# Performance work log

Measured on AMD Instinct MI355X. Metric: run time of the kernel, lower is better.

## Reference

```python
import jax, jax.numpy as jnp
import numpy as np
import math

B, D = 8192, 128
STEEPNESS = 1.0
TOPK_NEG = 10
N_SORT = TOPK_NEG + 1  # n_pos_augs - 1 + topk_neg = 1 + 10
EPS = 1e-8


def setup_inputs() -> dict:
    key = jax.random.key(0)
    k1, k2 = jax.random.split(key)
    aug1 = jax.random.normal(k1, (B, D), dtype=jnp.float32)
    aug2 = jax.random.normal(k2, (B, D), dtype=jnp.float32)
    return {"aug1": aug1, "aug2": aug2}


def _soft_sort_odd_even(x, steepness):
    """Differentiable odd-even transposition sort (diffsort, cauchy interpolation).
    x: [B, n]. Returns (sorted_x [B, n], P [B, n, n]) where sorted_x = x @ P and
    P[i, j] = relaxed probability that input element i lands at sorted position j."""
    b, n = x.shape
    P = jnp.broadcast_to(jnp.eye(n, dtype=x.dtype), (b, n, n))
    for layer in range(n):  # n layers, alternating even/odd pairs
        off = layer % 2
        idx_a = np.arange(off, n - 1, 2)
        idx_b = idx_a + 1
        a = x[:, idx_a]
        bb = x[:, idx_b]
        # cauchy CDF relaxation: alpha -> 1 when b > a (already ordered)
        alpha = jnp.arctan(steepness * (bb - a)) / math.pi + 0.5
        x = x.at[:, idx_a].set(alpha * a + (1.0 - alpha) * bb)
        x = x.at[:, idx_b].set((1.0 - alpha) * a + alpha * bb)
        Pa = P[:, :, idx_a]
        Pb = P[:, :, idx_b]
        al = alpha[:, None, :]
        P = P.at[:, :, idx_a].set(al * Pa + (1.0 - al) * Pb)
        P = P.at[:, :, idx_b].set((1.0 - al) * Pa + al * Pb)
    return x, P


def _bce(p, t):
    # torch.nn.BCELoss with log clamped at -100
    logp = jnp.clip(jnp.log(p), -100.0, None)
    log1mp = jnp.clip(jnp.log(1.0 - p), -100.0, None)
    return -jnp.mean(t * logp + (1.0 - t) * log1mp)


def _compute_loss(anchor, positive):
    anchor = anchor.astype(jnp.float32)
    positive = jax.lax.stop_gradient(positive.astype(jnp.float32))  # stop_grad=True
    # pairwise cosine similarity (dim=1)
    an = anchor / jnp.maximum(jnp.linalg.norm(anchor, axis=1, keepdims=True), EPS)
    pn = positive / jnp.maximum(jnp.linalg.norm(positive, axis=1, keepdims=True), EPS)
    pos_sims = jnp.sum(an * pn, axis=1, keepdims=True)  # [B, 1]; sort over dim=1 is a no-op
    # all-to-all cosine similarity vs detached anchors (negatives = anchor.detach())
    negs = jax.lax.stop_gradient(an)
    sim = an @ negs.T  # [B, B]
    nb = sim.shape[0]
    sim = jnp.where(jnp.eye(nb, dtype=bool), -jnp.inf, sim)  # mask self-similarity
    neg_top, _ = jax.lax.top_k(sim, TOPK_NEG)  # descending
    neg_top = neg_top[:, ::-1]                 # flip -> ascending
    sims = jnp.concatenate([neg_top, pos_sims], axis=1)  # [B, 11]
    _, P = _soft_sort_odd_even(sims, STEEPNESS)
    n = sims.shape[1]
    # perm_target = identity -> column-sum targets are first-k indicators
    p_neg = jnp.clip(jnp.sum(P[:, :, :TOPK_NEG], axis=2), 0.0, 1.0)  # [B, n]
    p_pos = jnp.clip(jnp.sum(P[:, :, TOPK_NEG:], axis=2), 0.0, 1.0)
    t_neg = jnp.broadcast_to((jnp.arange(n) < TOPK_NEG).astype(jnp.float32), (nb, n))
    t_pos = 1.0 - t_neg
    return 0.5 * (_bce(p_pos, t_pos) + _bce(p_neg, t_neg))


def reference(aug1, aug2):
    # n_augs = 2: each aug serves as anchor once, the other as the single positive
    loss1 = _compute_loss(aug1, aug2)
    loss2 = _compute_loss(aug2, aug1)
    return (loss1 + loss2) / 2.0
```

## Files before the change

### kernel.cpp

```cpp
#include <hip/hip_runtime.h>
#include <cstdint>
#include <cmath>

#define NB 8192
#define ND 128
#define CAP 48
#define CAPP 49
#define NEG_INF (-__builtin_inff())

typedef __attribute__((ext_vector_type(8))) __bf16 bf16x8;
typedef __attribute__((ext_vector_type(2))) __bf16 bf16x2;
typedef __attribute__((ext_vector_type(4))) float f32x4;


__device__ __forceinline__ void insert10(float t[10], float v) {
#pragma unroll
  for (int j = 0; j < 9; ++j) t[j] = __builtin_amdgcn_fmed3f(t[j], t[j + 1], v);
  t[9] = fmaxf(t[9], v);
}
__device__ __forceinline__ void insert11(float t[11], float v) {
#pragma unroll
  for (int j = 0; j < 10; ++j) t[j] = __builtin_amdgcn_fmed3f(t[j], t[j + 1], v);
  t[10] = fmaxf(t[10], v);
}

__device__ float row_loss(float x[11]) {
  float al[55];
#pragma unroll
  for (int layer = 0; layer < 11; ++layer) {
#pragma unroll
    for (int p = 0; p < 5; ++p) {
      int ii = (layer & 1) + 2 * p;
      float av = x[ii], bv = x[ii + 1];
      float a = atanf(bv - av) * 0.3183098861837907f + 0.5f;
      al[layer * 5 + p] = a;
      float be = 1.f - a;
      x[ii] = a * av + be * bv;
      x[ii + 1] = be * av + a * bv;
    }
  }
  float v[11];
#pragma unroll
  for (int i = 0; i < 11; ++i) v[i] = 0.f;
  v[10] = 1.f;
#pragma unroll
  for (int layer = 10; layer >= 0; --layer) {
#pragma unroll
    for (int p = 0; p < 5; ++p) {
      int ii = (layer & 1) + 2 * p;
      float a = al[layer * 5 + p];
      float be = 1.f - a;
      float va = v[ii], vb = v[ii + 1];
      v[ii] = a * va + be * vb;
      v[ii + 1] = be * va + a * vb;
    }
  }
  float C = fmaxf(logf(v[10]), -100.f);
#pragma unroll
  for (int i = 0; i < 10; ++i) C += fmaxf(logf(1.f - v[i]), -100.f);
  return C;
}

__global__ __launch_bounds__(256, 4) void knorm(const float* __restrict__ aug1,
                                                const float* __restrict__ aug2,
                                                __bf16* __restrict__ an,
                                                float* __restrict__ pos,
                                                float* __restrict__ out) {
  if (blockIdx.x == 0 && threadIdx.x == 0) out[0] = 0.f;
  int wid = threadIdx.x >> 6;
  int l = threadIdx.x & 63;
  int row = blockIdx.x * 4 + wid;
  const float2* a1 = (const float2*)(aug1) + (size_t)row * 64;
  const float2* a2 = (const float2*)(aug2) + (size_t)row * 64;
  float2 v1 = a1[l], v2 = a2[l];
  float ss1 = v1.x * v1.x + v1.y * v1.y;
  float ss2 = v2.x * v2.x + v2.y * v2.y;
  float dp = v1.x * v2.x + v1.y * v2.y;
#pragma unroll
  for (int off = 1; off < 64; off <<= 1) {
    ss1 += __shfl_xor(ss1, off);
    ss2 += __shfl_xor(ss2, off);
    dp += __shfl_xor(dp, off);
  }
  float inv1 = 1.0f / fmaxf(sqrtf(ss1), 1e-8f);
  float inv2 = 1.0f / fmaxf(sqrtf(ss2), 1e-8f);
  bf16x2 o1, o2;
  o1[0] = (__bf16)(v1.x * inv1);
  o1[1] = (__bf16)(v1.y * inv1);
  o2[0] = (__bf16)(v2.x * inv2);
  o2[1] = (__bf16)(v2.y * inv2);
  int unit = ((row >> 4) << 8) + ((l >> 4) << 6) + (((l >> 2) & 3) << 4) + (row & 15);
  ((bf16x2*)(an))[unit * 4 + (l & 3)] = o1;
  ((bf16x2*)(an + (size_t)NB * ND))[unit * 4 + (l & 3)] = o2;
  if (l == 0) pos[row] = dp * inv1 * inv2;
}

__global__ __launch_bounds__(256, 4) void kgram(const __bf16* __restrict__ an_all,
                                                float* __restrict__ tk,
                                                int* __restrict__ cnth,
                                                float* __restrict__ taug) {
  int dir = blockIdx.y;
  int rowg = blockIdx.x >> 2;
  int quar = blockIdx.x & 3;
  const bf16x8* an8 = (const bf16x8*)(an_all + (size_t)dir * NB * ND);
  int w = threadIdx.x >> 6;
  int l = threadIdx.x & 63;
  int q = l >> 4;
  int c = l & 15;
  int row_base = rowg * 64;
  const int col0 = quar * 2048;

  __shared__ float cand[64][CAPP];
  __shared__ int lcnt[64];
  __shared__ float sred[2][4];
  if (threadIdx.x < 64) lcnt[threadIdx.x] = 0;

  bf16x8 brow[4][4];
#pragma unroll
  for (int rb = 0; rb < 4; ++rb)
#pragma unroll
    for (int kc = 0; kc < 4; ++kc)
      brow[rb][kc] = an8[(size_t)row_base * 16 + rb * 256 + kc * 64 + l];

  const bf16x8* pf0 = an8 + ((size_t)col0 * 16 + w * 256 + l);
  bf16x8 a[4], a2[4];
  const f32x4 zz = {0.f, 0.f, 0.f, 0.f};
  f32x4 accA[4], accB[4];

  auto loadA = [&](int t) {
    const bf16x8* p = pf0 + (size_t)(t & 31) * 1024;
#pragma unroll
    for (int kc = 0; kc < 4; ++kc) a[kc] = p[kc * 64];
  };
  auto loadA2 = [&](int t) {
    const bf16x8* p = pf0 + (size_t)(t & 31) * 1024;
#pragma unroll
    for (int kc = 0; kc < 4; ++kc) a2[kc] = p[kc * 64];
  };
  auto mfma_tile = [&](f32x4* A, const bf16x8* src) {
#pragma unroll
    for (int rb = 0; rb < 4; ++rb)
      A[rb] = __builtin_amdgcn_mfma_f32_16x16x32_bf16(src[0], brow[rb][0], zz, 0, 0, 0);
#pragma unroll
    for (int kc = 1; kc < 4; ++kc)
#pragma unroll
      for (int rb = 0; rb < 4; ++rb)
        A[rb] = __builtin_amdgcn_mfma_f32_16x16x32_bf16(src[kc], brow[rb][kc], A[rb], 0, 0, 0);
  };
  auto consume = [&](const f32x4* acc, float tau) {
#pragma unroll
    for (int rb = 0; rb < 4; ++rb) {
      int rl = rb * 16 + c;
#pragma unroll
      for (int r = 0; r < 4; ++r) {
        float v = acc[rb][r];
        if (v > tau) {
          int s = atomicAdd(&lcnt[rl], 1);
          if (s < CAP) cand[rl][s] = v;
        }
      }
    }
  };

  loadA(0);
  mfma_tile(accA, a);
  loadA2(1);
  bool diag0 = (row_base == col0);
  float s1 = 0.f, s2 = 0.f;
#pragma unroll
  for (int rb = 0; rb < 4; ++rb) {
#pragma unroll
    for (int r = 0; r < 4; ++r) {
      float v = accA[rb][r];
      v = (diag0 && (w * 16 + q * 4 + r == rb * 16 + c)) ? 0.f : v;
      s1 += v;
      s2 = fmaf(v, v, s2);
    }
  }
#pragma unroll
  for (int off = 1; off < 64; off <<= 1) {
    s1 += __shfl_xor(s1, off);
    s2 += __shfl_xor(s2, off);
  }
  if (l == 0) { sred[0][w] = s1; sred[1][w] = s2; }
  __syncthreads();
  float n = diag0 ? 4032.f : 4096.f;
  float ts1 = sred[0][0] + sred[0][1] + sred[0][2] + sred[0][3];
  float ts2 = sred[1][0] + sred[1][1] + sred[1][2] + sred[1][3];
  float mu = ts1 / n;
  float sig = sqrtf(fmaxf(ts2 / n - mu * mu, 0.f));
  float tau = mu + 2.5f * sig;
  if (threadIdx.x == 0) taug[((size_t)dir * 128 + rowg) * 4 + quar] = tau;
  consume(accA, tau);

  mfma_tile(accA, a2);
  loadA(2);
  for (int t = 2; t < 32; t += 2) {
    mfma_tile(accB, a);
    loadA2(t + 1);
    consume(accA, tau);
    mfma_tile(accA, a2);
    loadA(t + 2);
    consume(accB, tau);
  }
  consume(accA, tau);

  __syncthreads();
  if (threadIdx.x < 64) {
    int rl = threadIdx.x;
    int cc = lcnt[rl];
    float t11[11];
#pragma unroll
    for (int j = 0; j < 11; ++j) t11[j] = NEG_INF;
    int m = cc < CAP ? cc : CAP;
    for (int i = 0; i < m; ++i) {
      float v = cand[rl][i];
      if (v > t11[0]) insert11(t11, v);
    }
    bool diagq = ((rowg >> 5) == quar);
    int row = row_base + rl;
    float* o = tk + ((size_t)(dir * NB + row) * 4 + quar) * 10;
    if (diagq) {
#pragma unroll
      for (int j = 0; j < 10; ++j) o[j] = t11[j];
    } else {
#pragma unroll
      for (int j = 0; j < 10; ++j) o[j] = t11[j + 1];
    }
    cnth[(size_t)(dir * NB + row) * 4 + quar] = cc;
  }
}

__global__ __launch_bounds__(64, 1) void ksort(const float* __restrict__ tk,
                                               const float* __restrict__ pos,
                                               const int* __restrict__ cnth,
                                               const float* __restrict__ taug,
                                               const __bf16* __restrict__ an_all,
                                               float* __restrict__ out) {
  int tid = blockIdx.x * 64 + threadIdx.x;
  int dir = tid >> 13;
  int row = tid & (NB - 1);
  int lane = threadIdx.x;

  const float* A = tk + (size_t)(dir * NB + row) * 40;
  float s10[10];
#pragma unroll
  for (int j = 0; j < 10; ++j) s10[j] = A[j];
#pragma unroll
  for (int h = 1; h < 4; ++h) {
#pragma unroll
    for (int j = 0; j < 10; ++j) {
      float v = A[h * 10 + j];
      if (v > s10[0]) insert10(s10, v);
    }
  }
  int rowg = row >> 6;
  const float* tg = taug + ((size_t)dir * 128 + rowg) * 4;
  float tmax = fmaxf(fmaxf(tg[0], tg[1]), fmaxf(tg[2], tg[3]));
  int4 cc4 = ((const int4*)cnth)[dir * NB + row];
  bool ok = (cc4.x <= CAP) && (cc4.y <= CAP) && (cc4.z <= CAP) &&
            (cc4.w <= CAP) && (s10[0] >= tmax);

  float C = 0.f;
  if (ok) {
    float x[11];
#pragma unroll
    for (int j = 0; j < 10; ++j) x[j] = s10[j];
    x[10] = pos[row];
    C = row_loss(x);
  }
#pragma unroll
  for (int off = 1; off < 64; off <<= 1) C += __shfl_xor(C, off);
  if (lane == 0) atomicAdd(out, C * (-1.f / (2.f * (float)NB * 11.f)));

  unsigned long long bad = __ballot(!ok);
  if (bad == 0ull) return;
  __shared__ float rv[128];
  __shared__ float lst[64][10];
  const __bf16* an = an_all + (size_t)dir * NB * ND;
  const bf16x8* an8 = (const bf16x8*)an;
  while (bad) {
    int b = __ffsll((long long)bad) - 1;
    bad &= bad - 1;
    int brow = (blockIdx.x * 64 + b) & (NB - 1);
    int u = ((brow >> 4) << 8) + ((lane >> 4) << 6) + (((lane >> 2) & 3) << 4) + (brow & 15);
    bf16x2 pr = ((const bf16x2*)an)[u * 4 + (lane & 3)];
    rv[lane * 2] = (float)pr[0];
    rv[lane * 2 + 1] = (float)pr[1];
    __syncthreads();
    float t10[10];
#pragma unroll
    for (int j = 0; j < 10; ++j) t10[j] = NEG_INF;
    for (int i = 0; i < 128; ++i) {
      int col = lane + i * 64;
      if (col == brow) continue;
      float d = 0.f;
#pragma unroll
      for (int j = 0; j < 16; ++j) {
        bf16x8 p = an8[(size_t)(col >> 4) * 256 + (j >> 2) * 64 + (j & 3) * 16 + (col & 15)];
        int kb = (j >> 2) * 32 + (j & 3) * 8;
#pragma unroll
        for (int e = 0; e < 8; ++e) d = fmaf(rv[kb + e], (float)p[e], d);
      }
      if (d > t10[0]) insert10(t10, d);
    }
#pragma unroll
    for (int j = 0; j < 10; ++j) lst[lane][j] = t10[j];
    __syncthreads();
    if (lane == 0) {
      float cur[10];
#pragma unroll
      for (int j = 0; j < 10; ++j) cur[j] = lst[0][j];
      for (int s = 1; s < 64; ++s)
        for (int j = 0; j < 10; ++j) {
          float v = lst[s][j];
          if (v > cur[0]) insert10(cur, v);
        }
      float x[11];
#pragma unroll
      for (int j = 0; j < 10; ++j) x[j] = cur[j];
      x[10] = pos[brow];
      atomicAdd(out, row_loss(x) * (-1.f / (2.f * (float)NB * 11.f)));
    }
    __syncthreads();
  }
}

extern "C" void kernel_launch(void* const* d_in, const int* in_sizes, int n_in,
                              void* d_out, int out_size, void* d_ws, size_t ws_size,
                              hipStream_t stream) {
  const float* aug1 = (const float*)d_in[0];
  const float* aug2 = (const float*)d_in[1];
  char* w = (char*)d_ws;
  __bf16* an = (__bf16*)w;
  float* pos = (float*)(w + (size_t)4 * 1024 * 1024);
  float* tk = pos + NB;
  int* cnth = (int*)(tk + (size_t)2 * NB * 40);
  float* taug = (float*)(cnth + (size_t)2 * NB * 4);

  knorm<<<dim3(NB / 4), dim3(256), 0, stream>>>(aug1, aug2, an, pos, (float*)d_out);
  kgram<<<dim3(512, 2), dim3(256), 0, stream>>>(an, tk, cnth, taug);
  ksort<<<dim3(2 * NB / 64), dim3(64), 0, stream>>>(tk, pos, cnth, taug, an, (float*)d_out);
}
```

Baseline: 112.0 us.

## Split per-row soft sort across 8 lanes and widen fallback top-k to 256 threads

The ksort kernel now gives each row 8 threads instead of one. Five of those lanes each own one comparator pair of the odd-even soft sort, exchange values through width-8 shuffles, and then run a backward pass that yields the probability vector for the BCE terms directly. The fallback brute-force top-10 path for rows that fail the cap check now spreads its column scan over 256 threads and merges the partial lists in two stages. This cuts serial per-thread sort work and raises occupancy, at the cost of 8x more threads and many shuffles per layer.

Result: slower. 141.0 us (+25.9%).

```diff
diff --git a/kernel.cpp b/kernel.cpp
--- a/kernel.cpp
+++ b/kernel.cpp
@@ -231,18 +231,19 @@
   }
 }
 
-__global__ __launch_bounds__(64, 1) void ksort(const float* __restrict__ tk,
-                                               const float* __restrict__ pos,
-                                               const int* __restrict__ cnth,
-                                               const float* __restrict__ taug,
-                                               const __bf16* __restrict__ an_all,
-                                               float* __restrict__ out) {
-  int tid = blockIdx.x * 64 + threadIdx.x;
-  int dir = tid >> 13;
-  int row = tid & (NB - 1);
-  int lane = threadIdx.x;
-
-  const float* A = tk + (size_t)(dir * NB + row) * 40;
+__global__ __launch_bounds__(256, 2) void ksort(const float* __restrict__ tk,
+                                                const float* __restrict__ pos,
+                                                const int* __restrict__ cnth,
+                                                const float* __restrict__ taug,
+                                                const __bf16* __restrict__ an_all,
+                                                float* __restrict__ out) {
+  int tid = blockIdx.x * 256 + threadIdx.x;
+  int rid = tid >> 3;
+  int sub = tid & 7;
+  int row = rid & (NB - 1);
+  int dir = rid >> 13;
+
+  const float* A = tk + (size_t)rid * 40;
   float s10[10];
 #pragma unroll
   for (int j = 0; j < 10; ++j) s10[j] = A[j];
@@ -257,72 +258,138 @@
   int rowg = row >> 6;
   const float* tg = taug + ((size_t)dir * 128 + rowg) * 4;
   float tmax = fmaxf(fmaxf(tg[0], tg[1]), fmaxf(tg[2], tg[3]));
-  int4 cc4 = ((const int4*)cnth)[dir * NB + row];
+  int4 cc4 = ((const int4*)cnth)[rid];
   bool ok = (cc4.x <= CAP) && (cc4.y <= CAP) && (cc4.z <= CAP) &&
             (cc4.w <= CAP) && (s10[0] >= tmax);
 
-  float C = 0.f;
-  if (ok) {
-    float x[11];
-#pragma unroll
-    for (int j = 0; j < 10; ++j) x[j] = s10[j];
-    x[10] = pos[row];
-    C = row_loss(x);
-  }
-#pragma unroll
-  for (int off = 1; off < 64; off <<= 1) C += __shfl_xor(C, off);
-  if (lane == 0) atomicAdd(out, C * (-1.f / (2.f * (float)NB * 11.f)));
-
-  unsigned long long bad = __ballot(!ok);
-  if (bad == 0ull) return;
+  float x[11];
+#pragma unroll
+  for (int j = 0; j < 10; ++j) x[j] = s10[j];
+  x[10] = pos[row];
+  int p = sub < 5 ? sub : sub - 5;
+  float al[11];
+#pragma unroll
+  for (int layer = 0; layer < 11; ++layer) {
+    int off = layer & 1;
+    int ii = off + 2 * p;
+    float av = x[ii], bv = x[ii + 1];
+    float a = atanf(bv - av) * 0.3183098861837907f + 0.5f;
+    al[layer] = a;
+    float be = 1.f - a;
+    float na = a * av + be * bv;
+    float nb = be * av + a * bv;
+#pragma unroll
+    for (int pp = 0; pp < 5; ++pp) {
+      x[off + 2 * pp] = __shfl(na, pp, 8);
+      x[off + 2 * pp + 1] = __shfl(nb, pp, 8);
+    }
+  }
+  float v[11];
+#pragma unroll
+  for (int i = 0; i < 11; ++i) v[i] = 0.f;
+  v[10] = 1.f;
+#pragma unroll
+  for (int layer = 10; layer >= 0; --layer) {
+    int off = layer & 1;
+    int ii = off + 2 * p;
+    float a = al[layer];
+    float be = 1.f - a;
+    float va = v[ii], vb = v[ii + 1];
+    float nva = a * va + be * vb;
+    float nvb = be * va + a * vb;
+#pragma unroll
+    for (int pp = 0; pp < 5; ++pp) {
+      v[off + 2 * pp] = __shfl(nva, pp, 8);
+      v[off + 2 * pp + 1] = __shfl(nvb, pp, 8);
+    }
+  }
+  float C = fmaxf(logf(v[10]), -100.f);
+#pragma unroll
+  for (int i = 0; i < 10; ++i) C += fmaxf(logf(1.f - v[i]), -100.f);
+
+  float contrib = (sub == 0 && ok) ? C : 0.f;
+#pragma unroll
+  for (int off = 1; off < 64; off <<= 1) contrib += __shfl_xor(contrib, off);
+  if ((threadIdx.x & 63) == 0)
+    atomicAdd(out, contrib * (-1.f / (2.f * (float)NB * 11.f)));
+
+  __shared__ unsigned long long badm[4];
+  unsigned long long bad = __ballot(sub == 0 && !ok);
+  if ((threadIdx.x & 63) == 0) badm[threadIdx.x >> 6] = bad;
+  __syncthreads();
+  unsigned long long anybad = badm[0] | badm[1] | badm[2] | badm[3];
+  if (anybad == 0ull) return;
+
   __shared__ float rv[128];
-  __shared__ float lst[64][10];
-  const __bf16* an = an_all + (size_t)dir * NB * ND;
+  __shared__ float lst[256][10];
+  int bdir = (blockIdx.x * 32) >> 13;
+  const __bf16* an = an_all + (size_t)bdir * NB * ND;
   const bf16x8* an8 = (const bf16x8*)an;
-  while (bad) {
-    int b = __ffsll((long long)bad) - 1;
-    bad &= bad - 1;
-    int brow = (blockIdx.x * 64 + b) & (NB - 1);
-    int u = ((brow >> 4) << 8) + ((lane >> 4) << 6) + (((lane >> 2) & 3) << 4) + (brow & 15);
-    bf16x2 pr = ((const bf16x2*)an)[u * 4 + (lane & 3)];
-    rv[lane * 2] = (float)pr[0];
-    rv[lane * 2 + 1] = (float)pr[1];
-    __syncthreads();
-    float t10[10];
-#pragma unroll
-    for (int j = 0; j < 10; ++j) t10[j] = NEG_INF;
-    for (int i = 0; i < 128; ++i) {
-      int col = lane + i * 64;
-      if (col == brow) continue;
-      float d = 0.f;
-#pragma unroll
-      for (int j = 0; j < 16; ++j) {
-        bf16x8 p = an8[(size_t)(col >> 4) * 256 + (j >> 2) * 64 + (j & 3) * 16 + (col & 15)];
-        int kb = (j >> 2) * 32 + (j & 3) * 8;
-#pragma unroll
-        for (int e = 0; e < 8; ++e) d = fmaf(rv[kb + e], (float)p[e], d);
+  for (int w2 = 0; w2 < 4; ++w2) {
+    unsigned long long m = badm[w2];
+    while (m) {
+      int b = __ffsll((long long)m) - 1;
+      m &= m - 1;
+      int brow = (blockIdx.x * 32 + w2 * 8 + (b >> 3)) & (NB - 1);
+      if (threadIdx.x < 64) {
+        int lane = threadIdx.x;
+        int u = ((brow >> 4) << 8) + ((lane >> 4) << 6) +
+                (((lane >> 2) & 3) << 4) + (brow & 15);
+        bf16x2 pr = ((const bf16x2*)an)[u * 4 + (lane & 3)];
+        rv[lane * 2] = (float)pr[0];
+        rv[lane * 2 + 1] = (float)pr[1];
       }
-      if (d > t10[0]) insert10(t10, d);
-    }
-#pragma unroll
-    for (int j = 0; j < 10; ++j) lst[lane][j] = t10[j];
-    __syncthreads();
-    if (lane == 0) {
-      float cur[10];
-#pragma unroll
-      for (int j = 0; j < 10; ++j) cur[j] = lst[0][j];
-      for (int s = 1; s < 64; ++s)
-        for (int j = 0; j < 10; ++j) {
-          float v = lst[s][j];
-          if (v > cur[0]) insert10(cur, v);
+      __syncthreads();
+      float t10[10];
+#pragma unroll
+      for (int j = 0; j < 10; ++j) t10[j] = NEG_INF;
+      for (int i = 0; i < 32; ++i) {
+        int col = threadIdx.x + i * 256;
+        if (col == brow) continue;
+        float d = 0.f;
+#pragma unroll
+        for (int j = 0; j < 16; ++j) {
+          bf16x8 pv = an8[(size_t)(col >> 4) * 256 + (j >> 2) * 64 +
+                          (j & 3) * 16 + (col & 15)];
+          int kb = (j >> 2) * 32 + (j & 3) * 8;
+#pragma unroll
+          for (int e = 0; e < 8; ++e) d = fmaf(rv[kb + e], (float)pv[e], d);
         }
-      float x[11];
-#pragma unroll
-      for (int j = 0; j < 10; ++j) x[j] = cur[j];
-      x[10] = pos[brow];
-      atomicAdd(out, row_loss(x) * (-1.f / (2.f * (float)NB * 11.f)));
-    }
-    __syncthreads();
+        if (d > t10[0]) insert10(t10, d);
+      }
+#pragma unroll
+      for (int j = 0; j < 10; ++j) lst[threadIdx.x][j] = t10[j];
+      __syncthreads();
+      if (threadIdx.x < 64) {
+        float cur[10];
+#pragma unroll
+        for (int j = 0; j < 10; ++j) cur[j] = lst[threadIdx.x][j];
+        for (int s = 64; s < 256; s += 64)
+          for (int j = 0; j < 10; ++j) {
+            float vv = lst[threadIdx.x + s][j];
+            if (vv > cur[0]) insert10(cur, vv);
+          }
+#pragma unroll
+        for (int j = 0; j < 10; ++j) lst[threadIdx.x][j] = cur[j];
+      }
+      __syncthreads();
+      if (threadIdx.x == 0) {
+        float cur[10];
+#pragma unroll
+        for (int j = 0; j < 10; ++j) cur[j] = lst[0][j];
+        for (int s = 1; s < 64; ++s)
+          for (int j = 0; j < 10; ++j) {
+            float vv = lst[s][j];
+            if (vv > cur[0]) insert10(cur, vv);
+          }
+        float xx[11];
+#pragma unroll
+        for (int j = 0; j < 10; ++j) xx[j] = cur[j];
+        xx[10] = pos[brow];
+        atomicAdd(out, row_loss(xx) * (-1.f / (2.f * (float)NB * 11.f)));
+      }
+      __syncthreads();
+    }
   }
 }
 
@@ -340,5 +407,5 @@
 
   knorm<<<dim3(NB / 4), dim3(256), 0, stream>>>(aug1, aug2, an, pos, (float*)d_out);
   kgram<<<dim3(512, 2), dim3(256), 0, stream>>>(an, tk, cnth, taug);
-  ksort<<<dim3(2 * NB / 64), dim3(64), 0, stream>>>(tk, pos, cnth, taug, an, (float*)d_out);
-}
+  ksort<<<dim3(512), dim3(256), 0, stream>>>(tk, pos, cnth, taug, an, (float*)d_out);
+}
```
